# Optimization experiments

Hardware: AMD Instinct MI355X
Metric: run time of the kernel (lower is better)

## Reference

```python
import jax, jax.numpy as jnp
import numpy as np

GRID = 128
N_PTS = 60000
K = 27


def _occupied_coords():
    # Deterministic blob-like occupancy: top-N voxels of a smooth random field.
    rng = np.random.RandomState(0)
    xs = np.arange(GRID, dtype=np.float32)
    X, Y, Z = np.meshgrid(xs, xs, xs, indexing='ij')
    f = np.zeros((GRID, GRID, GRID), np.float32)
    for _ in range(12):
        k = rng.uniform(0.04, 0.22, 3).astype(np.float32)
        ph = np.float32(rng.uniform(0, 2 * np.pi))
        a = np.float32(rng.randn())
        f += a * np.cos(k[0] * X + k[1] * Y + k[2] * Z + ph)
    idx = np.argpartition(f.ravel(), -N_PTS)[-N_PTS:]
    return np.stack(np.unravel_index(idx, f.shape), axis=1).astype(np.int64)


def _keys(c):
    return (c[:, 0] * GRID + c[:, 1]) * GRID + c[:, 2]


def _build_kmap(coords):
    # ME-style kernel map: for each of 27 offsets, pairs (input_row, output_row)
    # such that coord[out] + offset == coord[in]. Padded with index n (dummy row).
    n = coords.shape[0]
    key = _keys(coords)
    order = np.argsort(key)
    skey = key[order]
    ins, outs = [], []
    for dx in (-1, 0, 1):
        for dy in (-1, 0, 1):
            for dz in (-1, 0, 1):
                q = coords + np.array([dx, dy, dz], dtype=np.int64)
                valid = np.all((q >= 0) & (q < GRID), axis=1)
                qk = _keys(q)
                pos = np.clip(np.searchsorted(skey, qk), 0, n - 1)
                hit = valid & (skey[pos] == qk)
                ins.append(order[pos[hit]].astype(np.int32))
                outs.append(np.nonzero(hit)[0].astype(np.int32))
    m = max(len(a) for a in ins)
    in_idx = np.full((K, m), n, np.int32)
    out_idx = np.full((K, m), n, np.int32)
    for k in range(K):
        in_idx[k, : len(ins[k])] = ins[k]
        out_idx[k, : len(outs[k])] = outs[k]
    return jnp.asarray(in_idx), jnp.asarray(out_idx)


def setup_inputs() -> dict:
    coords = _occupied_coords()
    in1, out1 = _build_kmap(coords)
    pc, parent = np.unique(coords // 2, axis=0, return_inverse=True)  # maxpool k2 s2
    in2, out2 = _build_kmap(pc)
    n_pool = int(pc.shape[0])
    ks = jax.random.split(jax.random.key(0), 12)
    f32 = jnp.float32
    feats = jax.random.normal(ks[0], (N_PTS, 128), f32)
    W1 = jax.random.normal(ks[1], (K, 128, 128), f32) / np.sqrt(128 * K)
    W2 = jax.random.normal(ks[2], (K, 128, 256), f32) / np.sqrt(128 * K)
    W3 = jax.random.normal(ks[3], (K, 256, 256), f32) / np.sqrt(256 * K)
    W4 = jax.random.normal(ks[4], (K, 256, 256), f32) / np.sqrt(256 * K)
    g1 = 1.0 + 0.1 * jax.random.normal(ks[5], (128,), f32)
    b1 = 0.1 * jax.random.normal(ks[6], (128,), f32)
    g2 = 1.0 + 0.1 * jax.random.normal(ks[7], (256,), f32)
    b2 = 0.1 * jax.random.normal(ks[8], (256,), f32)
    g3 = 1.0 + 0.1 * jax.random.normal(ks[9], (256,), f32)
    b3 = 0.1 * jax.random.normal(ks[10], (256,), f32)
    return dict(feats=feats, W1=W1, g1=g1, b1=b1, W2=W2, g2=g2, b2=b2,
                W3=W3, g3=g3, b3=b3, W4=W4,
                in1=in1, out1=out1, in2=in2, out2=out2,
                parent=jnp.asarray(parent.astype(np.int32)), n_pool=n_pool)


def _sparse_conv(x, in_idx, out_idx, W, n_out):
    # x: [N_in, Cin]; in_idx/out_idx: [K, M] padded with N_in / n_out; W: [K, Cin, Cout]
    xp = jnp.concatenate([x, jnp.zeros((1, x.shape[1]), x.dtype)], axis=0)
    acc0 = jnp.zeros((n_out + 1, W.shape[2]), x.dtype)

    def step(acc, xs):
        i, o, Wk = xs
        return acc.at[o].add(xp[i] @ Wk), None

    acc, _ = jax.lax.scan(step, acc0, (in_idx, out_idx, W))
    return acc[:-1]


def _bn_relu(x, g, b):
    # training-mode BatchNorm over active voxels (ME applies BatchNorm1d to features)
    m = x.mean(0)
    v = x.var(0)
    return jax.nn.relu((x - m) * jax.lax.rsqrt(v + 1e-5) * g + b)


def reference(feats, W1, g1, b1, W2, g2, b2, W3, g3, b3, W4,
              in1, out1, in2, out2, parent, n_pool):
    n = feats.shape[0]
    x = _bn_relu(_sparse_conv(feats, in1, out1, W1, n), g1, b1)          # [N,128]
    x = jax.ops.segment_max(x, parent, num_segments=n_pool)             # maxpool 2x2x2/2
    x = _bn_relu(_sparse_conv(x, in2, out2, W2, n_pool), g2, b2)         # [Np,256]
    x = _bn_relu(_sparse_conv(x, in2, out2, W3, n_pool), g3, b3)         # [Np,256]
    return _sparse_conv(x, in2, out2, W4, n_pool)                        # [Np,256]
```

## Files before the change

### kernel.cpp

```cpp
#include <hip/hip_runtime.h>
#include <hip/hip_bf16.h>
#include <math.h>

#define K_OFF 27

typedef __attribute__((ext_vector_type(8))) short short8v;
typedef __attribute__((ext_vector_type(4))) float float4v;

static __device__ __forceinline__ unsigned short f2bf(float f) {
  __hip_bfloat16 h = __float2bfloat16(f);
  return *reinterpret_cast<unsigned short*>(&h);
}

static __device__ __forceinline__ void gload_lds16(const void* g, void* l) {
  __builtin_amdgcn_global_load_lds(
      (const __attribute__((address_space(1))) void*)g,
      (__attribute__((address_space(3))) void*)l, 16, 0, 0);
}

__global__ void fill_i32_kernel(int* __restrict__ p, int total, int val) {
  int i = blockIdx.x * blockDim.x + threadIdx.x;
  if (i < total) p[i] = val;
}

__global__ void build_table_kernel(const int* __restrict__ in_idx,
                                   const int* __restrict__ out_idx,
                                   int* __restrict__ table, int M, int n_valid,
                                   int n_out_pad) {
  int j = blockIdx.x * blockDim.x + threadIdx.x;
  if (j >= K_OFF * M) return;
  int k = j / M;
  int in = in_idx[j], out = out_idx[j];
  if (in < n_valid && out < n_valid) table[k * n_out_pad + out] = in;
}

__global__ void wtrans_kernel(const float* __restrict__ W,
                              unsigned short* __restrict__ Wt, int Cin,
                              int Cout) {
  __shared__ float t[32][33];
  const int k = blockIdx.z, ci0 = blockIdx.x * 32, co0 = blockIdx.y * 32;
  const float* Wk = W + (size_t)k * Cin * Cout;
  unsigned short* Wtk = Wt + (size_t)k * Cout * Cin;
#pragma unroll
  for (int i = 0; i < 4; ++i)
    t[threadIdx.y + i * 8][threadIdx.x] =
        Wk[(size_t)(ci0 + threadIdx.y + i * 8) * Cout + co0 + threadIdx.x];
  __syncthreads();
#pragma unroll
  for (int i = 0; i < 4; ++i)
    Wtk[(size_t)(co0 + threadIdx.y + i * 8) * Cin + ci0 + threadIdx.x] =
        f2bf(t[threadIdx.x][threadIdx.y + i * 8]);
}

__global__ void f32_to_bf16_kernel(const float* __restrict__ s,
                                   unsigned short* __restrict__ d, int total) {
  int i = (blockIdx.x * blockDim.x + threadIdx.x) * 4;
  if (i >= total) return;
  float4 v = *reinterpret_cast<const float4*>(s + i);
  ushort4 o = {f2bf(v.x), f2bf(v.y), f2bf(v.z), f2bf(v.w)};
  *reinterpret_cast<ushort4*>(d + i) = o;
}

template <int CIN>
__global__ __launch_bounds__(256) void spconv_mfma(
    const unsigned short* __restrict__ xb,
    const unsigned short* __restrict__ Wt,
    const int* __restrict__ table,
    float* __restrict__ y, int n_out, int n_out_pad, int Cout) {
  constexpr int BK = 32;
  constexpr int SPK = CIN / BK;
  const int S = K_OFF * SPK;

  __shared__ unsigned short As[2][128 * BK];
  __shared__ unsigned short Bs[2][128 * BK];
  __shared__ int idx_s[K_OFF * 128];

  const int tid = threadIdx.x;
  const int lane = tid & 63;
  const int wid = tid >> 6;
  const int row0 = blockIdx.x * 128;
  const int col0 = blockIdx.y * 128;
  const int wr = wid >> 1, wc = wid & 1;

  for (int j = tid; j < K_OFF * 128; j += 256)
    idx_s[j] = table[(j >> 7) * n_out_pad + row0 + (j & 127)];
  __syncthreads();

  const int srow = tid >> 2;
  const int sc4 = tid & 3;

  auto stage = [&](int buf, int s) {
    const int k = s / SPK;
    const int kk0 = (s % SPK) * BK;
    const int* idk = &idx_s[k << 7];
#pragma unroll
    for (int r = 0; r < 2; ++r) {
      const int row = r * 64 + srow;
      const int cg = sc4 ^ ((row >> 1) & 3);
      const int irow = idk[row];
      const unsigned short* srcA = xb + (size_t)irow * CIN + kk0 + cg * 8;
      gload_lds16(srcA, (void*)&As[buf][(r * 64 + wid * 16) * BK]);
      const unsigned short* srcB =
          Wt + ((size_t)k * Cout + col0 + row) * CIN + kk0 + cg * 8;
      gload_lds16(srcB, (void*)&Bs[buf][(r * 64 + wid * 16) * BK]);
    }
  };

  int a_off[4], b_off[4];
#pragma unroll
  for (int mi = 0; mi < 4; ++mi) {
    const int row = wr * 64 + mi * 16 + (lane & 15);
    const int ca = (lane >> 4) ^ ((row >> 1) & 3);
    a_off[mi] = row * BK + ca * 8;
    const int rowb = wc * 64 + mi * 16 + (lane & 15);
    const int cb = (lane >> 4) ^ ((rowb >> 1) & 3);
    b_off[mi] = rowb * BK + cb * 8;
  }

  float4v acc[4][4];
#pragma unroll
  for (int i = 0; i < 4; ++i)
#pragma unroll
    for (int j = 0; j < 4; ++j) acc[i][j] = (float4v)(0.f);

  stage(0, 0);
  for (int s = 0; s < S; ++s) {
    const int buf = s & 1;
    __syncthreads();
    if (s + 1 < S) stage(buf ^ 1, s + 1);
    short8v a[4], b[4];
#pragma unroll
    for (int i = 0; i < 4; ++i) {
      a[i] = *reinterpret_cast<const short8v*>(&As[buf][a_off[i]]);
      b[i] = *reinterpret_cast<const short8v*>(&Bs[buf][b_off[i]]);
    }
#pragma unroll
    for (int mi = 0; mi < 4; ++mi)
#pragma unroll
      for (int ni = 0; ni < 4; ++ni)
        acc[mi][ni] = __builtin_amdgcn_mfma_f32_16x16x32_bf16(
            a[mi], b[ni], acc[mi][ni], 0, 0, 0);
  }

#pragma unroll
  for (int mi = 0; mi < 4; ++mi) {
    const int rbase = row0 + wr * 64 + mi * 16 + ((lane >> 4) << 2);
#pragma unroll
    for (int ni = 0; ni < 4; ++ni) {
      const int col = col0 + wc * 64 + ni * 16 + (lane & 15);
#pragma unroll
      for (int j = 0; j < 4; ++j) {
        const int r = rbase + j;
        if (r < n_out) y[(size_t)r * Cout + col] = acc[mi][ni][j];
      }
    }
  }
}

__global__ void colstats_kernel(const float* __restrict__ y, int n, int C,
                                double* __restrict__ sums) {
  const int c = threadIdx.x;
  const int r0 = blockIdx.x * 64;
  const int r1 = min(r0 + 64, n);
  double s = 0.0, s2 = 0.0;
  for (int r = r0; r < r1; ++r) {
    float v = y[(size_t)r * C + c];
    s += v;
    s2 += (double)v * (double)v;
  }
  atomicAdd(&sums[c], s);
  atomicAdd(&sums[C + c], s2);
}

__global__ void finalize_kernel(const double* __restrict__ sums,
                                const float* __restrict__ g,
                                const float* __restrict__ b,
                                float* __restrict__ scale,
                                float* __restrict__ shift, int n, int C) {
  int c = blockIdx.x * blockDim.x + threadIdx.x;
  if (c >= C) return;
  double m = sums[c] / n;
  double v = sums[C + c] / n - m * m;
  float sc = (float)((double)g[c] / sqrt(v + 1e-5));
  scale[c] = sc;
  shift[c] = b[c] - (float)m * sc;
}

__global__ void bn_relu_pool_kernel(const float* __restrict__ y,
                                    const float* __restrict__ scale,
                                    const float* __restrict__ shift,
                                    const int* __restrict__ parent,
                                    unsigned int* __restrict__ pooled, int n,
                                    int C) {
  int i4 = (blockIdx.x * blockDim.x + threadIdx.x) * 4;
  if (i4 >= n * C) return;
  int r = i4 / C, c = i4 % C;
  float4 v = *reinterpret_cast<const float4*>(y + i4);
  float4 sc = *reinterpret_cast<const float4*>(scale + c);
  float4 sh = *reinterpret_cast<const float4*>(shift + c);
  unsigned int* dst = pooled + (size_t)parent[r] * C + c;
  atomicMax(dst + 0, __float_as_uint(fmaxf(fmaf(v.x, sc.x, sh.x), 0.f)));
  atomicMax(dst + 1, __float_as_uint(fmaxf(fmaf(v.y, sc.y, sh.y), 0.f)));
  atomicMax(dst + 2, __float_as_uint(fmaxf(fmaf(v.z, sc.z, sh.z), 0.f)));
  atomicMax(dst + 3, __float_as_uint(fmaxf(fmaf(v.w, sc.w, sh.w), 0.f)));
}

__global__ void bn_relu_bf16_kernel(const float* __restrict__ y,
                                    const float* __restrict__ scale,
                                    const float* __restrict__ shift,
                                    unsigned short* __restrict__ xb, int total,
                                    int C) {
  int i4 = (blockIdx.x * blockDim.x + threadIdx.x) * 4;
  if (i4 >= total) return;
  int c = i4 % C;
  float4 v = *reinterpret_cast<const float4*>(y + i4);
  float4 sc = *reinterpret_cast<const float4*>(scale + c);
  float4 sh = *reinterpret_cast<const float4*>(shift + c);
  ushort4 o = {f2bf(fmaxf(fmaf(v.x, sc.x, sh.x), 0.f)),
               f2bf(fmaxf(fmaf(v.y, sc.y, sh.y), 0.f)),
               f2bf(fmaxf(fmaf(v.z, sc.z, sh.z), 0.f)),
               f2bf(fmaxf(fmaf(v.w, sc.w, sh.w), 0.f))};
  *reinterpret_cast<ushort4*>(xb + i4) = o;
}

extern "C" void kernel_launch(void* const* d_in, const int* in_sizes, int n_in_,
                              void* d_out, int out_size, void* d_ws,
                              size_t ws_size, hipStream_t stream) {
  const float* feats = (const float*)d_in[0];
  const float* W1 = (const float*)d_in[1];
  const float* g1 = (const float*)d_in[2];
  const float* b1 = (const float*)d_in[3];
  const float* W2 = (const float*)d_in[4];
  const float* g2 = (const float*)d_in[5];
  const float* b2 = (const float*)d_in[6];
  const float* W3 = (const float*)d_in[7];
  const float* g3 = (const float*)d_in[8];
  const float* b3 = (const float*)d_in[9];
  const float* W4 = (const float*)d_in[10];
  const int* in1 = (const int*)d_in[11];
  const int* out1 = (const int*)d_in[12];
  const int* in2 = (const int*)d_in[13];
  const int* out2 = (const int*)d_in[14];
  const int* parent = (const int*)d_in[15];

  const int N1 = in_sizes[0] / 128;
  const int M1 = in_sizes[11] / K_OFF;
  const int M2 = in_sizes[13] / K_OFF;
  const int NP = out_size / 256;

  const int n1_blocks = (N1 + 127) / 128, n1_pad = n1_blocks * 128;
  const int np_blocks = (NP + 127) / 128, np_pad = np_blocks * 128;

  auto rnd = [](size_t v) { return (v + 255) & ~size_t(255); };
  auto mx = [](size_t a, size_t b) { return a > b ? a : b; };
  char* ws = (char*)d_ws;
  size_t off = 0;
  auto take = [&](size_t b) { void* p = ws + off; off += rnd(b); return p; };

  const size_t sz_y1 = (size_t)N1 * 128 * 4;
  const size_t sz_y23 = (size_t)NP * 256 * 4;
  const size_t sz_x1 = ((size_t)N1 + 1) * 128 * 2;
  const size_t sz_x23 = ((size_t)NP + 1) * 256 * 2;
  const size_t sz_t1 = (size_t)K_OFF * n1_pad * 4;
  const size_t sz_t2 = (size_t)K_OFF * np_pad * 4;
  const size_t sz_pool = (size_t)NP * 128 * 4;
  const size_t sz_poolbf = ((size_t)NP + 1) * 128 * 2;
  const size_t sz_wt2 = (size_t)K_OFF * 128 * 256 * 2;
  const size_t sz_wt34 = (size_t)K_OFF * 256 * 256 * 2;

  char* A = (char*)take(mx(rnd(sz_y1), 2 * rnd(sz_y23)));
  float* y1 = (float*)A;
  float* y2 = (float*)A;
  float* y3 = (float*)(A + rnd(sz_y23));
  char* B = (char*)take(
      mx(rnd(sz_x1), rnd(sz_wt2) + 2 * rnd(sz_wt34) + rnd(sz_poolbf)));
  unsigned short* x1b = (unsigned short*)B;
  unsigned short* Wt2 = (unsigned short*)B;
  unsigned short* Wt3 = (unsigned short*)(B + rnd(sz_wt2));
  unsigned short* Wt4 = (unsigned short*)(B + rnd(sz_wt2) + rnd(sz_wt34));
  unsigned short* poolbf =
      (unsigned short*)(B + rnd(sz_wt2) + 2 * rnd(sz_wt34));
  char* C = (char*)take(mx(rnd(sz_t1), mx(rnd(sz_pool), rnd(sz_x23))));
  int* table1 = (int*)C;
  float* pooled = (float*)C;
  unsigned short* x2b = (unsigned short*)C;
  unsigned short* x3b = (unsigned short*)C;
  int* table2 = (int*)take(sz_t2);
  unsigned short* Wt1 = (unsigned short*)take((size_t)K_OFF * 128 * 128 * 2);
  double* sums = (double*)take(3 * 512 * 8);
  double* sums1 = sums; double* sums2 = sums + 512; double* sums3 = sums + 1024;
  float* scsh = (float*)take(6 * 256 * 4);
  float* sc1 = scsh;        float* sh1 = scsh + 256;
  float* sc2 = scsh + 512;  float* sh2 = scsh + 768;
  float* sc3 = scsh + 1024; float* sh3 = scsh + 1280;

  dim3 wtb(32, 8);
  wtrans_kernel<<<dim3(4, 4, K_OFF), wtb, 0, stream>>>(W1, Wt1, 128, 128);

  f32_to_bf16_kernel<<<(N1 * 128 / 4 + 255) / 256, 256, 0, stream>>>(
      feats, x1b, N1 * 128);
  hipMemsetAsync(x1b + (size_t)N1 * 128, 0, 128 * 2, stream);

  fill_i32_kernel<<<(K_OFF * n1_pad + 255) / 256, 256, 0, stream>>>(
      table1, K_OFF * n1_pad, N1);
  fill_i32_kernel<<<(K_OFF * np_pad + 255) / 256, 256, 0, stream>>>(
      table2, K_OFF * np_pad, NP);
  build_table_kernel<<<(K_OFF * M1 + 255) / 256, 256, 0, stream>>>(
      in1, out1, table1, M1, N1, n1_pad);
  build_table_kernel<<<(K_OFF * M2 + 255) / 256, 256, 0, stream>>>(
      in2, out2, table2, M2, NP, np_pad);
  hipMemsetAsync(sums, 0, 3 * 512 * 8, stream);

  spconv_mfma<128><<<dim3(n1_blocks, 1), 256, 0, stream>>>(
      x1b, Wt1, table1, y1, N1, n1_pad, 128);
  colstats_kernel<<<(N1 + 63) / 64, 128, 0, stream>>>(y1, N1, 128, sums1);
  finalize_kernel<<<1, 128, 0, stream>>>(sums1, g1, b1, sc1, sh1, N1, 128);
  wtrans_kernel<<<dim3(4, 8, K_OFF), wtb, 0, stream>>>(W2, Wt2, 128, 256);
  wtrans_kernel<<<dim3(8, 8, K_OFF), wtb, 0, stream>>>(W3, Wt3, 256, 256);
  wtrans_kernel<<<dim3(8, 8, K_OFF), wtb, 0, stream>>>(W4, Wt4, 256, 256);
  hipMemsetAsync(pooled, 0, sz_pool, stream);
  bn_relu_pool_kernel<<<((N1 * 128 / 4) + 255) / 256, 256, 0, stream>>>(
      y1, sc1, sh1, parent, (unsigned int*)pooled, N1, 128);
  f32_to_bf16_kernel<<<((NP * 128 / 4) + 255) / 256, 256, 0, stream>>>(
      pooled, poolbf, NP * 128);
  hipMemsetAsync(poolbf + (size_t)NP * 128, 0, 128 * 2, stream);

  spconv_mfma<128><<<dim3(np_blocks, 2), 256, 0, stream>>>(
      poolbf, Wt2, table2, y2, NP, np_pad, 256);
  colstats_kernel<<<(NP + 63) / 64, 256, 0, stream>>>(y2, NP, 256, sums2);
  finalize_kernel<<<1, 256, 0, stream>>>(sums2, g2, b2, sc2, sh2, NP, 256);
  bn_relu_bf16_kernel<<<((NP * 256 / 4) + 255) / 256, 256, 0, stream>>>(
      y2, sc2, sh2, x2b, NP * 256, 256);
  hipMemsetAsync(x2b + (size_t)NP * 256, 0, 256 * 2, stream);

  spconv_mfma<256><<<dim3(np_blocks, 2), 256, 0, stream>>>(
      x2b, Wt3, table2, y3, NP, np_pad, 256);
  colstats_kernel<<<(NP + 63) / 64, 256, 0, stream>>>(y3, NP, 256, sums3);
  finalize_kernel<<<1, 256, 0, stream>>>(sums3, g3, b3, sc3, sh3, NP, 256);
  bn_relu_bf16_kernel<<<((NP * 256 / 4) + 255) / 256, 256, 0, stream>>>(
      y3, sc3, sh3, x3b, NP * 256, 256);
  hipMemsetAsync(x3b + (size_t)NP * 256, 0, 256 * 2, stream);

  spconv_mfma<256><<<dim3(np_blocks, 2), 256, 0, stream>>>(
      x3b, Wt4, table2, (float*)d_out, NP, np_pad, 256);
}
```

Before: 827.8 us.

## Split sparse conv kernel offsets across grid z with atomic accumulation

Result: faster. 769.7 us (-7.0%).

```diff
diff --git a/kernel.cpp b/kernel.cpp
--- a/kernel.cpp
+++ b/kernel.cpp
@@ -61,7 +61,7 @@
   *reinterpret_cast<ushort4*>(d + i) = o;
 }
 
-template <int CIN>
+template <int CIN, int KPG>
 __global__ __launch_bounds__(256) void spconv_mfma(
     const unsigned short* __restrict__ xb,
     const unsigned short* __restrict__ Wt,
@@ -69,30 +69,31 @@
     float* __restrict__ y, int n_out, int n_out_pad, int Cout) {
   constexpr int BK = 32;
   constexpr int SPK = CIN / BK;
-  const int S = K_OFF * SPK;
+  constexpr int S = KPG * SPK;
 
   __shared__ unsigned short As[2][128 * BK];
   __shared__ unsigned short Bs[2][128 * BK];
-  __shared__ int idx_s[K_OFF * 128];
+  __shared__ int idx_s[KPG * 128];
 
   const int tid = threadIdx.x;
   const int lane = tid & 63;
   const int wid = tid >> 6;
   const int row0 = blockIdx.x * 128;
   const int col0 = blockIdx.y * 128;
+  const int kbase = blockIdx.z * KPG;
   const int wr = wid >> 1, wc = wid & 1;
 
-  for (int j = tid; j < K_OFF * 128; j += 256)
-    idx_s[j] = table[(j >> 7) * n_out_pad + row0 + (j & 127)];
+  for (int j = tid; j < KPG * 128; j += 256)
+    idx_s[j] = table[(kbase + (j >> 7)) * n_out_pad + row0 + (j & 127)];
   __syncthreads();
 
   const int srow = tid >> 2;
   const int sc4 = tid & 3;
 
   auto stage = [&](int buf, int s) {
-    const int k = s / SPK;
+    const int kl = s / SPK;
     const int kk0 = (s % SPK) * BK;
-    const int* idk = &idx_s[k << 7];
+    const int* idk = &idx_s[kl << 7];
 #pragma unroll
     for (int r = 0; r < 2; ++r) {
       const int row = r * 64 + srow;
@@ -101,7 +102,7 @@
       const unsigned short* srcA = xb + (size_t)irow * CIN + kk0 + cg * 8;
       gload_lds16(srcA, (void*)&As[buf][(r * 64 + wid * 16) * BK]);
       const unsigned short* srcB =
-          Wt + ((size_t)k * Cout + col0 + row) * CIN + kk0 + cg * 8;
+          Wt + ((size_t)(kbase + kl) * Cout + col0 + row) * CIN + kk0 + cg * 8;
       gload_lds16(srcB, (void*)&Bs[buf][(r * 64 + wid * 16) * BK]);
     }
   };
@@ -151,7 +152,7 @@
 #pragma unroll
       for (int j = 0; j < 4; ++j) {
         const int r = rbase + j;
-        if (r < n_out) y[(size_t)r * Cout + col] = acc[mi][ni][j];
+        if (r < n_out) atomicAdd(&y[(size_t)r * Cout + col], acc[mi][ni][j]);
       }
     }
   }
@@ -311,7 +312,8 @@
       in2, out2, table2, M2, NP, np_pad);
   hipMemsetAsync(sums, 0, 3 * 512 * 8, stream);
 
-  spconv_mfma<128><<<dim3(n1_blocks, 1), 256, 0, stream>>>(
+  hipMemsetAsync(y1, 0, sz_y1, stream);
+  spconv_mfma<128, 9><<<dim3(n1_blocks, 1, 3), 256, 0, stream>>>(
       x1b, Wt1, table1, y1, N1, n1_pad, 128);
   colstats_kernel<<<(N1 + 63) / 64, 128, 0, stream>>>(y1, N1, 128, sums1);
   finalize_kernel<<<1, 128, 0, stream>>>(sums1, g1, b1, sc1, sh1, N1, 128);
@@ -325,7 +327,8 @@
       pooled, poolbf, NP * 128);
   hipMemsetAsync(poolbf + (size_t)NP * 128, 0, 128 * 2, stream);
 
-  spconv_mfma<128><<<dim3(np_blocks, 2), 256, 0, stream>>>(
+  hipMemsetAsync(y2, 0, sz_y23, stream);
+  spconv_mfma<128, 3><<<dim3(np_blocks, 2, 9), 256, 0, stream>>>(
       poolbf, Wt2, table2, y2, NP, np_pad, 256);
   colstats_kernel<<<(NP + 63) / 64, 256, 0, stream>>>(y2, NP, 256, sums2);
   finalize_kernel<<<1, 256, 0, stream>>>(sums2, g2, b2, sc2, sh2, NP, 256);
@@ -333,7 +336,8 @@
       y2, sc2, sh2, x2b, NP * 256, 256);
   hipMemsetAsync(x2b + (size_t)NP * 256, 0, 256 * 2, stream);
 
-  spconv_mfma<256><<<dim3(np_blocks, 2), 256, 0, stream>>>(
+  hipMemsetAsync(y3, 0, sz_y23, stream);
+  spconv_mfma<256, 3><<<dim3(np_blocks, 2, 9), 256, 0, stream>>>(
       x2b, Wt3, table2, y3, NP, np_pad, 256);
   colstats_kernel<<<(NP + 63) / 64, 256, 0, stream>>>(y3, NP, 256, sums3);
   finalize_kernel<<<1, 256, 0, stream>>>(sums3, g3, b3, sc3, sh3, NP, 256);
@@ -341,6 +345,7 @@
       y3, sc3, sh3, x3b, NP * 256, 256);
   hipMemsetAsync(x3b + (size_t)NP * 256, 0, 256 * 2, stream);
 
-  spconv_mfma<256><<<dim3(np_blocks, 2), 256, 0, stream>>>(
+  hipMemsetAsync(d_out, 0, (size_t)out_size * 4, stream);
+  spconv_mfma<256, 3><<<dim3(np_blocks, 2, 9), 256, 0, stream>>>(
       x3b, Wt4, table2, (float*)d_out, NP, np_pad, 256);
 }
```
